# Performance work log

Hardware: AMD Instinct MI355X
Metric: run time of the kernel (lower is better)

Reference implementation:

```python
import jax, jax.numpy as jnp
import numpy as np

B, N, E = 256, 50000, 128000


def setup_inputs() -> dict:
    key = jax.random.key(0)
    ks = jax.random.split(key, 12)
    # forward args (normalized predictions / demand truth)
    pred_p_norm = jax.random.normal(ks[0], (B, N), dtype=jnp.float32)
    pred_f_norm = jax.random.normal(ks[1], (B, E), dtype=jnp.float32)
    true_d_norm = jax.random.normal(ks[2], (B, N), dtype=jnp.float32)
    # scaler params (positive scales)
    p_mean = jax.random.normal(ks[3], (N,), dtype=jnp.float32) * 10.0 + 50.0
    p_scale = jax.random.uniform(ks[4], (N,), dtype=jnp.float32, minval=0.5, maxval=5.0)
    f_mean = jax.random.normal(ks[5], (E,), dtype=jnp.float32) * 0.1
    f_scale = jax.random.uniform(ks[6], (E,), dtype=jnp.float32, minval=0.01, maxval=1.0)
    d_mean = jax.random.normal(ks[7], (N,), dtype=jnp.float32) * 0.01
    d_scale = jax.random.uniform(ks[8], (N,), dtype=jnp.float32, minval=0.001, maxval=0.1)
    node_elevation = jax.random.uniform(ks[9], (N,), dtype=jnp.float32, minval=0.0, maxval=300.0)
    # edge static attrs -> Hazen-Williams resistance R = 10.67 * L * (C+eps)^-1.852 * (D+eps)^-4.87
    L = jax.random.uniform(ks[10], (E,), dtype=jnp.float32, minval=10.0, maxval=1000.0)
    D = jax.random.uniform(ks[11], (E,), dtype=jnp.float32, minval=0.05, maxval=1.0)
    C = jnp.full((E,), 130.0, dtype=jnp.float32)
    eps = 1e-06
    R = 10.67 * L * (C + eps) ** (-1.852) * (D + eps) ** (-4.87)
    edge_index = jax.random.randint(jax.random.fold_in(key, 99), (2, E), 0, N, dtype=jnp.int32)
    return {
        'pred_p_norm': pred_p_norm, 'pred_f_norm': pred_f_norm, 'true_d_norm': true_d_norm,
        'p_mean': p_mean, 'p_scale': p_scale, 'f_mean': f_mean, 'f_scale': f_scale,
        'd_mean': d_mean, 'd_scale': d_scale, 'node_elevation': node_elevation,
        'R': R, 'edge_index': edge_index,
    }


def reference(pred_p_norm, pred_f_norm, true_d_norm, p_mean, p_scale, f_mean, f_scale,
              d_mean, d_scale, node_elevation, R, edge_index):
    n_nodes = pred_p_norm.shape[1]
    # denormalize (broadcast per-node / per-edge scalers over batch)
    P = pred_p_norm * p_scale[None, :] + p_mean[None, :]          # [B, N]
    Q = pred_f_norm * f_scale[None, :] + f_mean[None, :]          # [B, E]
    d = true_d_norm * d_scale[None, :] + d_mean[None, :]          # [B, N]
    H = P + node_elevation[None, :]                               # hydraulic head [B, N]
    src, dst = edge_index[0], edge_index[1]
    # mass conservation: net inflow per node vs demand
    Q_T = Q.T                                                      # [E, B]
    q_out = jax.ops.segment_sum(Q_T, src, num_segments=n_nodes).T  # [B, N]
    q_in = jax.ops.segment_sum(Q_T, dst, num_segments=n_nodes).T   # [B, N]
    q_net = q_in - q_out
    loss_mass = jnp.mean((q_net - d) ** 2)
    # head loss (Hazen-Williams): delta_h vs R*Q*|Q|^0.852
    h_src = H[:, src]                                              # [B, E]
    h_dst = H[:, dst]                                              # [B, E]
    delta_h_pred = h_src - h_dst
    friction_slope = R[None, :] * Q * jnp.abs(Q) ** 0.852
    loss_head = jnp.mean((delta_h_pred - friction_slope) ** 2)
    return (loss_mass, loss_head)
```

## Files before the change

kernel.cpp:

```cpp
#include <hip/hip_runtime.h>
#include <hip/hip_fp16.h>

#define TILE 64
#define CAP 32

__global__ void k_zero(int* __restrict__ p, int n) {
    const int i = blockIdx.x * 256 + threadIdx.x;
    if (i < n) p[i] = 0;
}

__global__ void k_build_ht(const float* __restrict__ pred_p,
                           const float* __restrict__ p_scale,
                           const float* __restrict__ p_mean,
                           const float* __restrict__ elev,
                           const float* __restrict__ true_d,
                           const float* __restrict__ d_scale,
                           const float* __restrict__ d_mean,
                           __half* __restrict__ HTh,
                           __half* __restrict__ TD,
                           int B, int N) {
    __shared__ __align__(16) float tile[TILE][TILE + 2];
    const int n0 = blockIdx.x * TILE;
    const int b0 = blockIdx.y * TILE;
    const int tn = threadIdx.x % TILE;
    const int tw = threadIdx.x / TILE;
    const int c  = threadIdx.x & 31;
    const int rg = threadIdx.x >> 5;
    const int n = n0 + tn;

    {
        float sc = 0.f, mn = 0.f, el = 0.f;
        if (n < N) { sc = p_scale[n]; mn = p_mean[n]; el = elev[n]; }
        #pragma unroll
        for (int i = 0; i < TILE / 4; ++i) {
            const int bl = i * 4 + tw;
            float v = 0.f;
            if (n < N) v = pred_p[(size_t)(b0 + bl) * N + n] * sc + mn + el;
            tile[tn][bl] = v;
        }
        __syncthreads();
        #pragma unroll
        for (int i = 0; i < 8; ++i) {
            const int nl = i * 8 + rg;
            const int nn = n0 + nl;
            if (nn < N) {
                const float2 f = *reinterpret_cast<const float2*>(&tile[nl][2 * c]);
                reinterpret_cast<__half2*>(HTh + (size_t)nn * B + b0)[c] =
                    __floats2half2_rn(f.x, f.y);
            }
        }
    }
    __syncthreads();
    {
        float sc = 0.f, mn = 0.f;
        if (n < N) { sc = d_scale[n]; mn = d_mean[n]; }
        #pragma unroll
        for (int i = 0; i < TILE / 4; ++i) {
            const int bl = i * 4 + tw;
            float v = 0.f;
            if (n < N) v = true_d[(size_t)(b0 + bl) * N + n] * sc + mn;
            tile[tn][bl] = v;
        }
        __syncthreads();
        #pragma unroll
        for (int i = 0; i < 8; ++i) {
            const int nl = i * 8 + rg;
            const int nn = n0 + nl;
            if (nn < N) {
                const float2 f = *reinterpret_cast<const float2*>(&tile[nl][2 * c]);
                reinterpret_cast<__half2*>(TD + (size_t)nn * B + b0)[c] =
                    __floats2half2_rn(f.x, f.y);
            }
        }
    }
}

__global__ void k_fill(const int* __restrict__ esrc, const int* __restrict__ edst,
                       int* __restrict__ cnt, int* __restrict__ bucket, int E) {
    const int e = blockIdx.x * 256 + threadIdx.x;
    if (e < E) {
        const int s = esrc[e];
        const int ps = atomicAdd(&cnt[s], 1);
        if (ps < CAP) bucket[(size_t)s * CAP + ps] = (e << 1);
        const int d = edst[e];
        const int pd = atomicAdd(&cnt[d], 1);
        if (pd < CAP) bucket[(size_t)d * CAP + pd] = (e << 1) | 1;
    }
}

__global__ __launch_bounds__(256) void k_edges(
        const float* __restrict__ pred_f,
        const float* __restrict__ f_scale,
        const float* __restrict__ f_mean,
        const float* __restrict__ Rcoef,
        const int* __restrict__ esrc,
        const int* __restrict__ edst,
        const __half* __restrict__ HTh,
        __half* __restrict__ QT,
        double* __restrict__ headp,
        int B, int E) {
    __shared__ __align__(16) __half qth[TILE][66];
    __shared__ double wsum[4];
    const int e0 = blockIdx.x * TILE;
    const int b0 = blockIdx.y * TILE;
    const int tn = threadIdx.x & 63;
    const int tw = threadIdx.x >> 6;

    const int e = e0 + tn;
    const float fs = f_scale[e];
    const float fm = f_mean[e];

    #pragma unroll
    for (int i = 0; i < 16; ++i) {
        const int bl = i * 4 + tw;
        const float v = pred_f[(size_t)(b0 + bl) * E + e] * fs + fm;
        qth[tn][bl] = __float2half_rn(v);
    }
    __syncthreads();

    float hs[16], hd[16], Rv[16];
    #pragma unroll
    for (int j = 0; j < 16; ++j) {
        const int ee = e0 + tw * 16 + j;
        const int s = esrc[ee];
        const int d = edst[ee];
        Rv[j] = Rcoef[ee];
        hs[j] = __half2float(HTh[(size_t)s * 256 + b0 + tn]);
        hd[j] = __half2float(HTh[(size_t)d * 256 + b0 + tn]);
    }

    const int sel = tn >> 5;
    const int pc  = tn & 31;
    #pragma unroll
    for (int k = 0; k < 8; ++k) {
        const int el = tw * 16 + 2 * k + sel;
        const int ee = e0 + el;
        const __half2 h = *reinterpret_cast<const __half2*>(&qth[el][2 * pc]);
        *reinterpret_cast<__half2*>(QT + (size_t)ee * 256 + b0 + 2 * pc) = h;
    }

    double head = 0.0;
    #pragma unroll
    for (int j = 0; j < 16; ++j) {
        const int el = tw * 16 + j;
        const float q = __half2float(qth[el][tn]);
        const float aq = fabsf(q);
        const float pw = exp2f(0.852f * __log2f(aq));
        const float fr = Rv[j] * q * pw;
        const float t = (hs[j] - hd[j]) - fr;
        head += (double)t * (double)t;
    }

    #pragma unroll
    for (int off = 32; off >= 1; off >>= 1)
        head += __shfl_down(head, off, 64);
    if ((threadIdx.x & 63) == 0) wsum[threadIdx.x >> 6] = head;
    __syncthreads();
    if (threadIdx.x == 0)
        headp[(size_t)blockIdx.y * gridDim.x + blockIdx.x] =
            wsum[0] + wsum[1] + wsum[2] + wsum[3];
}

__global__ __launch_bounds__(256) void k_nodemass(
        const __half* __restrict__ QT,
        const __half* __restrict__ TD,
        const int* __restrict__ cnt,
        const int* __restrict__ bucket,
        double* __restrict__ massp,
        int N) {
    __shared__ double wsum[4];
    const int w = threadIdx.x >> 6;
    const int lane = threadIdx.x & 63;
    const int n = blockIdx.x * 4 + w;

    double m = 0.0;
    if (n < N) {
        const uint2 tdr = *reinterpret_cast<const uint2*>(
            (const char*)TD + (size_t)n * 512 + (size_t)lane * 8);

        int deg = cnt[n];
        if (deg > CAP) deg = CAP;
        const int* brow = bucket + (size_t)n * CAP;

        float qn0 = 0.f, qn1 = 0.f, qn2 = 0.f, qn3 = 0.f;
        if (deg <= 4) {
            int   ivv[4];
            float sg[4];
            uint2 vv[4];
            #pragma unroll
            for (int u = 0; u < 4; ++u) {
                const int kk = (u < deg) ? u : (deg > 0 ? deg - 1 : 0);
                ivv[u] = (deg > 0) ? brow[kk] : 0;
                sg[u] = (u < deg) ? ((ivv[u] & 1) ? 1.f : -1.f) : 0.f;
                vv[u] = *reinterpret_cast<const uint2*>(
                    (const char*)QT + (size_t)(ivv[u] >> 1) * 512
                                    + (size_t)lane * 8);
            }
            #pragma unroll
            for (int u = 0; u < 4; ++u) {
                const __half2 a = *reinterpret_cast<const __half2*>(&vv[u].x);
                const __half2 b = *reinterpret_cast<const __half2*>(&vv[u].y);
                const float2 fa = __half22float2(a);
                const float2 fb = __half22float2(b);
                qn0 += sg[u] * fa.x; qn1 += sg[u] * fa.y;
                qn2 += sg[u] * fb.x; qn3 += sg[u] * fb.y;
            }
        } else {
            for (int k = 0; k < deg; k += 8) {
                int   ivv[8];
                float sg[8];
                uint2 vv[8];
                #pragma unroll
                for (int u = 0; u < 8; ++u) {
                    const int kk = (k + u < deg) ? (k + u) : (deg - 1);
                    ivv[u] = brow[kk];
                    sg[u] = (k + u < deg) ? ((ivv[u] & 1) ? 1.f : -1.f) : 0.f;
                    vv[u] = *reinterpret_cast<const uint2*>(
                        (const char*)QT + (size_t)(ivv[u] >> 1) * 512
                                        + (size_t)lane * 8);
                }
                #pragma unroll
                for (int u = 0; u < 8; ++u) {
                    const __half2 a = *reinterpret_cast<const __half2*>(&vv[u].x);
                    const __half2 b = *reinterpret_cast<const __half2*>(&vv[u].y);
                    const float2 fa = __half22float2(a);
                    const float2 fb = __half22float2(b);
                    qn0 += sg[u] * fa.x; qn1 += sg[u] * fa.y;
                    qn2 += sg[u] * fb.x; qn3 += sg[u] * fb.y;
                }
            }
        }

        const __half2 d01 = *reinterpret_cast<const __half2*>(&tdr.x);
        const __half2 d23 = *reinterpret_cast<const __half2*>(&tdr.y);
        const float2 f01 = __half22float2(d01);
        const float2 f23 = __half22float2(d23);
        const float t0 = qn0 - f01.x;
        const float t1 = qn1 - f01.y;
        const float t2 = qn2 - f23.x;
        const float t3 = qn3 - f23.y;
        m = (double)t0 * t0 + (double)t1 * t1
          + (double)t2 * t2 + (double)t3 * t3;
    }

    #pragma unroll
    for (int off = 32; off >= 1; off >>= 1)
        m += __shfl_down(m, off, 64);
    if (lane == 0) wsum[w] = m;
    __syncthreads();
    if (threadIdx.x == 0)
        massp[blockIdx.x] = wsum[0] + wsum[1] + wsum[2] + wsum[3];
}

__global__ void k_reduce(const double* __restrict__ massp, int nm,
                         const double* __restrict__ headp, int nh,
                         float* __restrict__ out,
                         double inv_mass, double inv_head) {
    __shared__ double sh[256];
    const int t = threadIdx.x;

    double s = 0.0;
    for (int i = t; i < nm; i += 256) s += massp[i];
    sh[t] = s;
    __syncthreads();
    #pragma unroll
    for (int off = 128; off >= 1; off >>= 1) {
        if (t < off) sh[t] += sh[t + off];
        __syncthreads();
    }
    double mass_total = 0.0;
    if (t == 0) mass_total = sh[0];
    __syncthreads();

    s = 0.0;
    for (int i = t; i < nh; i += 256) s += headp[i];
    sh[t] = s;
    __syncthreads();
    #pragma unroll
    for (int off = 128; off >= 1; off >>= 1) {
        if (t < off) sh[t] += sh[t + off];
        __syncthreads();
    }
    if (t == 0) {
        out[0] = (float)(mass_total * inv_mass);
        out[1] = (float)(sh[0] * inv_head);
    }
}

static inline size_t align256s(size_t x) { return (x + 255) & ~(size_t)255; }

extern "C" void kernel_launch(void* const* d_in, const int* in_sizes, int n_in,
                              void* d_out, int out_size, void* d_ws, size_t ws_size,
                              hipStream_t stream) {
    const float* pred_p  = (const float*)d_in[0];
    const float* pred_f  = (const float*)d_in[1];
    const float* true_d  = (const float*)d_in[2];
    const float* p_mean  = (const float*)d_in[3];
    const float* p_scale = (const float*)d_in[4];
    const float* f_mean  = (const float*)d_in[5];
    const float* f_scale = (const float*)d_in[6];
    const float* d_mean  = (const float*)d_in[7];
    const float* d_scale = (const float*)d_in[8];
    const float* elev    = (const float*)d_in[9];
    const float* Rcoef   = (const float*)d_in[10];
    const int*   eidx    = (const int*)d_in[11];

    const int N = in_sizes[3];
    const int E = in_sizes[10];
    const int B = in_sizes[0] / N;

    const int* esrc = eidx;
    const int* edst = eidx + E;

    const int gn = (N + TILE - 1) / TILE;
    const int gb = B / TILE;
    const int ge = E / TILE;
    const int nbk = (N + 255) / 256;
    const int nmB = (N + 3) / 4;

    char* ws = (char*)d_ws;
    size_t off = 0;
    __half* HTh   = (__half*)(ws + off); off = align256s(off + (size_t)N * B * 2);
    __half* TD    = (__half*)(ws + off); off = align256s(off + (size_t)N * B * 2);
    __half* QT    = (__half*)(ws + off); off = align256s(off + (size_t)E * B * 2);
    int* bucket   = (int*)(ws + off);    off = align256s(off + (size_t)N * CAP * 4);
    double* headp = (double*)(ws + off); off = align256s(off + (size_t)ge * gb * 8);
    double* massp = (double*)(ws + off); off = align256s(off + (size_t)nmB * 8);
    int* cnt      = (int*)(ws + off);    off = align256s(off + (size_t)N * 4);

    k_zero<<<nbk, 256, 0, stream>>>(cnt, N);
    k_fill<<<(E + 255) / 256, 256, 0, stream>>>(esrc, edst, cnt, bucket, E);

    k_build_ht<<<dim3(gn, gb), 256, 0, stream>>>(pred_p, p_scale, p_mean, elev,
                                                 true_d, d_scale, d_mean,
                                                 HTh, TD, B, N);
    k_edges<<<dim3(ge, gb), 256, 0, stream>>>(pred_f, f_scale, f_mean, Rcoef,
                                              esrc, edst, HTh, QT, headp, B, E);
    k_nodemass<<<nmB, 256, 0, stream>>>(QT, TD, cnt, bucket, massp, N);
    k_reduce<<<1, 256, 0, stream>>>(massp, nmB, headp, ge * gb,
                                    (float*)d_out,
                                    1.0 / ((double)B * (double)N),
                                    1.0 / ((double)B * (double)E));
}
```

Baseline: 163.9 us.

## Gather node heads via direct global-to-LDS loads with 128-wide batch tiles

The edge kernel now handles 128 batch columns per block instead of 64, halving the grid's y dimension. The per-edge gathers of src/dst head values go through global_load_lds straight into shared memory as 4-byte half2 pairs instead of scalar half register loads, and the QT store and head computation work on half2 pairs. The aim is fewer, wider gather transactions and less per-edge index and coefficient reloading across batch tiles, at the cost of more LDS per block (which may lower occupancy). The gather loads are issued before the pred_f transpose so their latency overlaps it. The hardcoded grid of 2 assumes B=256.

```diff
diff --git a/kernel.cpp b/kernel.cpp
--- a/kernel.cpp
+++ b/kernel.cpp
@@ -3,6 +3,11 @@
 
 #define TILE 64
 #define CAP 32
+
+#define GLOAD_LDS(gptr, lptr, sz)                                              \
+    __builtin_amdgcn_global_load_lds(                                          \
+        (const __attribute__((address_space(1))) unsigned int*)(gptr),         \
+        (__attribute__((address_space(3))) unsigned int*)(lptr), (sz), 0, 0)
 
 __global__ void k_zero(int* __restrict__ p, int n) {
     const int i = blockIdx.x * 256 + threadIdx.x;
@@ -99,10 +104,12 @@
         __half* __restrict__ QT,
         double* __restrict__ headp,
         int B, int E) {
-    __shared__ __align__(16) __half qth[TILE][66];
+    __shared__ __align__(16) __half qth[TILE][130];
+    __shared__ __align__(16) __half hsb[4][16][128];
+    __shared__ __align__(16) __half hdb[4][16][128];
     __shared__ double wsum[4];
     const int e0 = blockIdx.x * TILE;
-    const int b0 = blockIdx.y * TILE;
+    const int b0 = blockIdx.y * 128;
     const int tn = threadIdx.x & 63;
     const int tw = threadIdx.x >> 6;
 
@@ -110,45 +117,60 @@
     const float fs = f_scale[e];
     const float fm = f_mean[e];
 
-    #pragma unroll
-    for (int i = 0; i < 16; ++i) {
-        const int bl = i * 4 + tw;
-        const float v = pred_f[(size_t)(b0 + bl) * E + e] * fs + fm;
-        qth[tn][bl] = __float2half_rn(v);
-    }
-    __syncthreads();
-
-    float hs[16], hd[16], Rv[16];
+    float Rv[16];
     #pragma unroll
     for (int j = 0; j < 16; ++j) {
         const int ee = e0 + tw * 16 + j;
         const int s = esrc[ee];
         const int d = edst[ee];
         Rv[j] = Rcoef[ee];
-        hs[j] = __half2float(HTh[(size_t)s * 256 + b0 + tn]);
-        hd[j] = __half2float(HTh[(size_t)d * 256 + b0 + tn]);
-    }
-
-    const int sel = tn >> 5;
-    const int pc  = tn & 31;
-    #pragma unroll
-    for (int k = 0; k < 8; ++k) {
-        const int el = tw * 16 + 2 * k + sel;
-        const int ee = e0 + el;
-        const __half2 h = *reinterpret_cast<const __half2*>(&qth[el][2 * pc]);
-        *reinterpret_cast<__half2*>(QT + (size_t)ee * 256 + b0 + 2 * pc) = h;
-    }
-
-    double head = 0.0;
+        GLOAD_LDS(HTh + (size_t)s * 256 + b0 + 2 * tn, &hsb[tw][j][0], 4);
+        GLOAD_LDS(HTh + (size_t)d * 256 + b0 + 2 * tn, &hdb[tw][j][0], 4);
+    }
+
+    for (int i = 0; i < 32; ++i) {
+        const int row = tw * 32 + i;
+        const float v = pred_f[(size_t)(b0 + row) * E + e] * fs + fm;
+        qth[tn][row] = __float2half_rn(v);
+    }
+    __syncthreads();
+
     #pragma unroll
     for (int j = 0; j < 16; ++j) {
         const int el = tw * 16 + j;
-        const float q = __half2float(qth[el][tn]);
-        const float aq = fabsf(q);
-        const float pw = exp2f(0.852f * __log2f(aq));
-        const float fr = Rv[j] * q * pw;
-        const float t = (hs[j] - hd[j]) - fr;
-        head += (double)t * (double)t;
+        const int ee = e0 + el;
+        const unsigned int u = *reinterpret_cast<const unsigned int*>(
+            &qth[el][2 * tn]);
+        *reinterpret_cast<unsigned int*>(
+            QT + (size_t)ee * 256 + b0 + 2 * tn) = u;
+    }
+
+    double head = 0.0;
+    #pragma unroll
+    for (int j = 0; j < 16; ++j) {
+        const int el = tw * 16 + j;
+        const unsigned int qu = *reinterpret_cast<const unsigned int*>(
+            &qth[el][2 * tn]);
+        const unsigned int su = *reinterpret_cast<const unsigned int*>(
+            &hsb[tw][j][2 * tn]);
+        const unsigned int du = *reinterpret_cast<const unsigned int*>(
+            &hdb[tw][j][2 * tn]);
+        const float2 qf = __half22float2(*reinterpret_cast<const __half2*>(&qu));
+        const float2 sf = __half22float2(*reinterpret_cast<const __half2*>(&su));
+        const float2 df = __half22float2(*reinterpret_cast<const __half2*>(&du));
+        const float R = Rv[j];
+        {
+            const float q = qf.x;
+            const float pw = exp2f(0.852f * __log2f(fabsf(q)));
+            const float t = (sf.x - df.x) - R * q * pw;
+            head += (double)t * (double)t;
+        }
+        {
+            const float q = qf.y;
+            const float pw = exp2f(0.852f * __log2f(fabsf(q)));
+            const float t = (sf.y - df.y) - R * q * pw;
+            head += (double)t * (double)t;
+        }
     }
 
     #pragma unroll
@@ -324,7 +346,7 @@
     __half* TD    = (__half*)(ws + off); off = align256s(off + (size_t)N * B * 2);
     __half* QT    = (__half*)(ws + off); off = align256s(off + (size_t)E * B * 2);
     int* bucket   = (int*)(ws + off);    off = align256s(off + (size_t)N * CAP * 4);
-    double* headp = (double*)(ws + off); off = align256s(off + (size_t)ge * gb * 8);
+    double* headp = (double*)(ws + off); off = align256s(off + (size_t)2 * ge * 8);
     double* massp = (double*)(ws + off); off = align256s(off + (size_t)nmB * 8);
     int* cnt      = (int*)(ws + off);    off = align256s(off + (size_t)N * 4);
 
@@ -334,10 +356,10 @@
     k_build_ht<<<dim3(gn, gb), 256, 0, stream>>>(pred_p, p_scale, p_mean, elev,
                                                  true_d, d_scale, d_mean,
                                                  HTh, TD, B, N);
-    k_edges<<<dim3(ge, gb), 256, 0, stream>>>(pred_f, f_scale, f_mean, Rcoef,
-                                              esrc, edst, HTh, QT, headp, B, E);
+    k_edges<<<dim3(ge, 2), 256, 0, stream>>>(pred_f, f_scale, f_mean, Rcoef,
+                                             esrc, edst, HTh, QT, headp, B, E);
     k_nodemass<<<nmB, 256, 0, stream>>>(QT, TD, cnt, bucket, massp, N);
-    k_reduce<<<1, 256, 0, stream>>>(massp, nmB, headp, ge * gb,
+    k_reduce<<<1, 256, 0, stream>>>(massp, nmB, headp, 2 * ge,
                                     (float*)d_out,
                                     1.0 / ((double)B * (double)N),
                                     1.0 / ((double)B * (double)E));
```

Result: no change. 162.7 us (-0.7%).
